# Kernel tuning notes

Measured on AMD Instinct MI355X. Metric: run time of the kernel, lower is better.

The kernel has to match this reference:

```python
import jax, jax.numpy as jnp
import numpy as np

N_NODES = 80_000
D_IN = 128
D_HID = 128
D_EMB = 64
N_EDGES = 2_560_000
NUM_PEAKS = 40_000
N_TF = 128
N_GENE = 8_000
MLP_HID = 128
N_OUT = 2


def setup_inputs() -> dict:
    key = jax.random.key(0)
    ks = jax.random.split(key, 8)
    x = jax.random.normal(ks[0], (N_NODES, D_IN), jnp.float32)
    edge_index = jax.random.randint(ks[1], (2, N_EDGES), 0, N_NODES)
    tf_index_list = jax.random.randint(ks[2], (N_TF,), 0, N_NODES - NUM_PEAKS)
    gene_index_list = jax.random.randint(ks[3], (N_GENE,), 0, N_NODES - NUM_PEAKS)
    s = lambda k, shp, fan: jax.random.normal(k, shp, jnp.float32) * np.float32(1.0 / np.sqrt(fan))
    W1 = s(ks[4], (D_IN, D_HID), D_IN)
    b1 = jnp.zeros((D_HID,), jnp.float32)
    W2 = s(ks[5], (D_HID, D_EMB), D_HID)
    b2 = jnp.zeros((D_EMB,), jnp.float32)
    Wm1 = s(ks[6], (2 * D_EMB, MLP_HID), 2 * D_EMB)
    bm1 = jnp.zeros((MLP_HID,), jnp.float32)
    Wm2 = s(ks[7], (MLP_HID, N_OUT), MLP_HID)
    bm2 = jnp.zeros((N_OUT,), jnp.float32)
    return dict(x=x, W1=W1, b1=b1, W2=W2, b2=b2, Wm1=Wm1, bm1=bm1, Wm2=Wm2, bm2=bm2,
                edge_index=edge_index, num=NUM_PEAKS,
                tf_index_list=tf_index_list, gene_index_list=gene_index_list)


def _gcn_agg(h, src, dst, n):
    # mean aggregation of neighbor features: agg[i] = mean_{(j->i) in E} h[j]
    deg = jax.ops.segment_sum(jnp.ones((src.shape[0],), h.dtype), dst, num_segments=n)
    agg = jax.ops.segment_sum(h[src], dst, num_segments=n)
    return agg / jnp.maximum(deg, 1.0)[:, None]


def reference(x, W1, b1, W2, b2, Wm1, bm1, Wm2, bm2,
              edge_index, num, tf_index_list, gene_index_list):
    src, dst = edge_index[0], edge_index[1]
    n = x.shape[0]
    # 2-layer GCN (mean aggregation) -> node embeddings [N, D_EMB]
    h = jax.nn.relu(_gcn_agg(x, src, dst, n) @ W1 + b1)
    emb = _gcn_agg(h, src, dst, n) @ W2 + b2
    # split_tensor(emb, num): pX = emb[:num] (unused), gX = emb[num:]
    gX = emb[num:]
    tf_emb = gX[tf_index_list]      # [T, d]
    g_emb = gX[gene_index_list]     # [G, d]
    T, d = tf_emb.shape
    G = g_emb.shape[0]
    # vectorized equivalent of the nested (tf, gene) concat loop; row order = tf*G + g
    combined = jnp.concatenate([
        jnp.broadcast_to(tf_emb[:, None, :], (T, G, d)),
        jnp.broadcast_to(g_emb[None, :, :], (T, G, d)),
    ], axis=-1).reshape(T * G, 2 * d)
    hid = jax.nn.relu(combined @ Wm1 + bm1)
    out = hid @ Wm2 + bm2
    return jax.nn.softmax(out, axis=-1)
```

## Files before the change

### kernel.cpp

```cpp
#include <hip/hip_runtime.h>
#include <math.h>

#define DIM 128
#define DEMB 64
#define CHUNK 8192


__device__ __forceinline__ unsigned pack_bf16x2(float a, float b) {
    unsigned ua = __float_as_uint(a);
    unsigned ub = __float_as_uint(b);
    ua = (ua + 0x7fffu + ((ua >> 16) & 1u)) >> 16;
    ub = (ub + 0x7fffu + ((ub >> 16) & 1u)) & 0xffff0000u;
    return ua | ub;
}
__device__ __forceinline__ float lo_bf16(unsigned v) { return __uint_as_float(v << 16); }
__device__ __forceinline__ float hi_bf16(unsigned v) { return __uint_as_float(v & 0xffff0000u); }


__global__ __launch_bounds__(256) void convert_kernel(const float* __restrict__ in,
                                                      unsigned* __restrict__ out, int n2) {
    int i = blockIdx.x * 256 + threadIdx.x;
    int stride = gridDim.x * 256;
    for (; i < n2; i += stride) {
        float2 v = reinterpret_cast<const float2*>(in)[i];
        out[i] = pack_bf16x2(v.x, v.y);
    }
}


__global__ __launch_bounds__(256) void bucket_count(const int* __restrict__ dst,
                                                    int* __restrict__ bcnt,
                                                    int n_edges, int nbuck) {
    __shared__ int h[384];
    for (int i = threadIdx.x; i < nbuck; i += 256) h[i] = 0;
    __syncthreads();
    int i = blockIdx.x * 256 + threadIdx.x;
    int stride = gridDim.x * 256;
    for (; i < n_edges; i += stride) atomicAdd(&h[dst[i] >> 8], 1);
    __syncthreads();
    for (int i2 = threadIdx.x; i2 < nbuck; i2 += 256)
        if (h[i2]) atomicAdd(&bcnt[i2], h[i2]);
}

__global__ __launch_bounds__(512) void bucket_scan(const int* __restrict__ bcnt,
                                                   int* __restrict__ bstart,
                                                   int* __restrict__ bcursor,
                                                   int nbuck, int n_edges) {
    __shared__ int sm[512];
    int tid = threadIdx.x;
    int v = (tid < nbuck) ? bcnt[tid] : 0;
    sm[tid] = v;
    __syncthreads();
    for (int off = 1; off < 512; off <<= 1) {
        int t = (tid >= off) ? sm[tid - off] : 0;
        __syncthreads();
        if (tid >= off) sm[tid] += t;
        __syncthreads();
    }
    if (tid < nbuck) {
        int e = sm[tid] - v;
        bstart[tid] = e;
        bcursor[tid] = e;
    }
    if (tid == 0) bstart[nbuck] = n_edges;
}

__global__ __launch_bounds__(256) void bucket_scatter(const int* __restrict__ src,
                                                      const int* __restrict__ dst,
                                                      int* __restrict__ bcursor,
                                                      unsigned* __restrict__ binned,
                                                      int n_edges, int nbuck) {
    __shared__ int cnt[384], off[384], gbase[384], cur[384];
    __shared__ unsigned stage[CHUNK];
    int tid = threadIdx.x;
    int e0 = blockIdx.x * CHUNK;
    int ne = min(CHUNK, n_edges - e0);
    for (int i = tid; i < nbuck; i += 256) cnt[i] = 0;
    __syncthreads();
    for (int j = tid; j < ne; j += 256) atomicAdd(&cnt[dst[e0 + j] >> 8], 1);
    __syncthreads();
    if (tid == 0) {
        int s = 0;
        for (int b = 0; b < nbuck; b++) { off[b] = s; s += cnt[b]; }
    }
    __syncthreads();
    for (int b = tid; b < nbuck; b += 256) {
        cur[b] = off[b];
        gbase[b] = cnt[b] ? atomicAdd(&bcursor[b], cnt[b]) : 0;
    }
    __syncthreads();
    for (int j = tid; j < ne; j += 256) {
        int d = dst[e0 + j];
        int s = src[e0 + j];
        int b = d >> 8;
        int p = atomicAdd(&cur[b], 1);
        stage[p] = ((unsigned)s << 8) | (unsigned)(d & 255);
    }
    __syncthreads();
    int wv = tid >> 6, lane = tid & 63;
    for (int b = wv; b < nbuck; b += 4) {
        int c = cnt[b], o = off[b], g = gbase[b];
        for (int k = lane; k < c; k += 64) binned[g + k] = stage[o + k];
    }
}

__global__ __launch_bounds__(256) void bucket_csr(const unsigned* __restrict__ binned,
                                                  const int* __restrict__ bstart,
                                                  int* __restrict__ counts,
                                                  int* __restrict__ rowstart,
                                                  int* __restrict__ ssorted,
                                                  int n_nodes) {
    __shared__ int sm[256], cur[256];
    __shared__ int cntv[256];
    int b = blockIdx.x;
    int bs = bstart[b], be = bstart[b + 1];
    int node0 = b << 8;
    int tid = threadIdx.x;
    cntv[tid] = 0;
    __syncthreads();
    for (int j = bs + tid; j < be; j += 256) atomicAdd(&cntv[binned[j] & 255u], 1);
    __syncthreads();
    int v = cntv[tid];
    sm[tid] = v;
    __syncthreads();
    for (int off = 1; off < 256; off <<= 1) {
        int t = (tid >= off) ? sm[tid - off] : 0;
        __syncthreads();
        if (tid >= off) sm[tid] += t;
        __syncthreads();
    }
    int excl = sm[tid] - v;
    int node = node0 + tid;
    if (node < n_nodes) {
        counts[node] = v;
        rowstart[node] = bs + excl;
    }
    cur[tid] = excl;
    __syncthreads();
    for (int j = bs + tid; j < be; j += 256) {
        unsigned e = binned[j];
        int p = atomicAdd(&cur[(int)(e & 255u)], 1);
        ssorted[bs + p] = (int)(e >> 8);
    }
}


__global__ __launch_bounds__(256) void agg_kernel(const unsigned* __restrict__ xh,
                                                  const int* __restrict__ rowstart,
                                                  const int* __restrict__ counts,
                                                  const int* __restrict__ ssorted,
                                                  float* __restrict__ A, int n_nodes) {
    int wave = (blockIdx.x * 256 + threadIdx.x) >> 6;
    int lane = threadIdx.x & 63;
    if (wave >= n_nodes) return;
    int base = rowstart[wave];
    int deg = counts[wave];
    const unsigned* xp = xh + lane;
    float ax = 0.f, ay = 0.f;
    int j = 0;
    for (; j + 8 <= deg; j += 8) {
        int s0 = ssorted[base + j];
        int s1 = ssorted[base + j + 1];
        int s2 = ssorted[base + j + 2];
        int s3 = ssorted[base + j + 3];
        int s4 = ssorted[base + j + 4];
        int s5 = ssorted[base + j + 5];
        int s6 = ssorted[base + j + 6];
        int s7 = ssorted[base + j + 7];
        unsigned v0 = xp[(size_t)s0 * 64];
        unsigned v1 = xp[(size_t)s1 * 64];
        unsigned v2 = xp[(size_t)s2 * 64];
        unsigned v3 = xp[(size_t)s3 * 64];
        unsigned v4 = xp[(size_t)s4 * 64];
        unsigned v5 = xp[(size_t)s5 * 64];
        unsigned v6 = xp[(size_t)s6 * 64];
        unsigned v7 = xp[(size_t)s7 * 64];
        ax += ((lo_bf16(v0) + lo_bf16(v1)) + (lo_bf16(v2) + lo_bf16(v3))) +
              ((lo_bf16(v4) + lo_bf16(v5)) + (lo_bf16(v6) + lo_bf16(v7)));
        ay += ((hi_bf16(v0) + hi_bf16(v1)) + (hi_bf16(v2) + hi_bf16(v3))) +
              ((hi_bf16(v4) + hi_bf16(v5)) + (hi_bf16(v6) + hi_bf16(v7)));
    }
    for (; j < deg; j++) {
        int s = ssorted[base + j];
        unsigned v = xp[(size_t)s * 64];
        ax += lo_bf16(v);
        ay += hi_bf16(v);
    }
    float inv = 1.f / fmaxf((float)deg, 1.f);
    float2 st = {ax * inv, ay * inv};
    *reinterpret_cast<float2*>(A + (size_t)wave * DIM + 2 * lane) = st;
}


__global__ __launch_bounds__(256) void gemm1_kernel(const float* __restrict__ A,
                                                    const float* __restrict__ W1,
                                                    const float* __restrict__ b1,
                                                    unsigned* __restrict__ Hh, int n_rows) {
    __shared__ float W1s[DIM * DIM];
    __shared__ float As[32 * DIM];
    int tid = threadIdx.x;
    for (int i = 0; i < 16; i++) {
        int idx = (i * 256 + tid) * 4;
        *reinterpret_cast<float4*>(&W1s[idx]) = *reinterpret_cast<const float4*>(&W1[idx]);
    }
    int r0 = blockIdx.x * 32;
    for (int i = 0; i < 4; i++) {
        int idx = (i * 256 + tid) * 4;
        int gr = r0 + (idx >> 7);
        float4 vv = {0, 0, 0, 0};
        if (gr < n_rows) vv = *reinterpret_cast<const float4*>(&A[(size_t)r0 * DIM + idx]);
        *reinterpret_cast<float4*>(&As[idx]) = vv;
    }
    __syncthreads();
    int tx = tid & 31, ty = tid >> 5;
    float4 b = *reinterpret_cast<const float4*>(&b1[tx * 4]);
    float acc[4][4];
#pragma unroll
    for (int i = 0; i < 4; i++) {
        acc[i][0] = b.x; acc[i][1] = b.y; acc[i][2] = b.z; acc[i][3] = b.w;
    }
#pragma unroll 8
    for (int kc = 0; kc < 32; kc++) {
        int k = kc * 4;
        float4 w0 = *reinterpret_cast<const float4*>(&W1s[(k + 0) * DIM + tx * 4]);
        float4 w1 = *reinterpret_cast<const float4*>(&W1s[(k + 1) * DIM + tx * 4]);
        float4 w2 = *reinterpret_cast<const float4*>(&W1s[(k + 2) * DIM + tx * 4]);
        float4 w3 = *reinterpret_cast<const float4*>(&W1s[(k + 3) * DIM + tx * 4]);
#pragma unroll
        for (int i = 0; i < 4; i++) {
            float4 a = *reinterpret_cast<const float4*>(&As[(ty * 4 + i) * DIM + k]);
            acc[i][0] += a.x * w0.x; acc[i][1] += a.x * w0.y; acc[i][2] += a.x * w0.z; acc[i][3] += a.x * w0.w;
            acc[i][0] += a.y * w1.x; acc[i][1] += a.y * w1.y; acc[i][2] += a.y * w1.z; acc[i][3] += a.y * w1.w;
            acc[i][0] += a.z * w2.x; acc[i][1] += a.z * w2.y; acc[i][2] += a.z * w2.z; acc[i][3] += a.z * w2.w;
            acc[i][0] += a.w * w3.x; acc[i][1] += a.w * w3.y; acc[i][2] += a.w * w3.z; acc[i][3] += a.w * w3.w;
        }
    }
#pragma unroll
    for (int i = 0; i < 4; i++) {
        int r = r0 + ty * 4 + i;
        if (r < n_rows) {
            float o0 = fmaxf(acc[i][0], 0.f);
            float o1 = fmaxf(acc[i][1], 0.f);
            float o2 = fmaxf(acc[i][2], 0.f);
            float o3 = fmaxf(acc[i][3], 0.f);
            uint2 pk = {pack_bf16x2(o0, o1), pack_bf16x2(o2, o3)};
            *reinterpret_cast<uint2*>(&Hh[(size_t)r * 64 + tx * 2]) = pk;
        }
    }
}


__global__ __launch_bounds__(256) void target_kernel(const unsigned* __restrict__ Hh,
                                                     const float* __restrict__ W2,
                                                     const float* __restrict__ b2,
                                                     const int* __restrict__ rowstart,
                                                     const int* __restrict__ counts,
                                                     const int* __restrict__ ssorted,
                                                     const int* __restrict__ dnum,
                                                     const int* __restrict__ tf_idx,
                                                     const int* __restrict__ gene_idx,
                                                     float* __restrict__ emb, int T, int ntar) {
    __shared__ float W2s[DIM * DEMB];
    __shared__ float aggS[4][DIM];
    int tid = threadIdx.x;
    for (int i = 0; i < 8; i++) {
        int idx = (i * 256 + tid) * 4;
        *reinterpret_cast<float4*>(&W2s[idx]) = *reinterpret_cast<const float4*>(&W2[idx]);
    }
    int wv = tid >> 6, lane = tid & 63;
    int i = blockIdx.x * 4 + wv;
    int num = dnum[0];
    if (i < ntar) {
        int idx = (i < T) ? tf_idx[i] : gene_idx[i - T];
        int node = num + idx;
        int base = rowstart[node];
        int deg = counts[node];
        const unsigned* hp = Hh + lane;
        float ax = 0.f, ay = 0.f;
        int j = 0;
        for (; j + 4 <= deg; j += 4) {
            int s0 = ssorted[base + j];
            int s1 = ssorted[base + j + 1];
            int s2 = ssorted[base + j + 2];
            int s3 = ssorted[base + j + 3];
            unsigned v0 = hp[(size_t)s0 * 64];
            unsigned v1 = hp[(size_t)s1 * 64];
            unsigned v2 = hp[(size_t)s2 * 64];
            unsigned v3 = hp[(size_t)s3 * 64];
            ax += (lo_bf16(v0) + lo_bf16(v1)) + (lo_bf16(v2) + lo_bf16(v3));
            ay += (hi_bf16(v0) + hi_bf16(v1)) + (hi_bf16(v2) + hi_bf16(v3));
        }
        for (; j < deg; j++) {
            int s = ssorted[base + j];
            unsigned v = hp[(size_t)s * 64];
            ax += lo_bf16(v);
            ay += hi_bf16(v);
        }
        float inv = 1.f / fmaxf((float)deg, 1.f);
        float2 st = {ax * inv, ay * inv};
        *reinterpret_cast<float2*>(&aggS[wv][2 * lane]) = st;
    }
    __syncthreads();
    if (i < ntar) {
        float e = b2[lane];
#pragma unroll 4
        for (int k = 0; k < DIM; k++) e += aggS[wv][k] * W2s[k * DEMB + lane];
        emb[(size_t)i * DEMB + lane] = e;
    }
}


__global__ __launch_bounds__(128) void ab_kernel(const float* __restrict__ emb,
                                                 const float* __restrict__ Wm1,
                                                 const float* __restrict__ bm1,
                                                 float* __restrict__ AB, int T, int ntar) {
    int i = blockIdx.x;
    int j = threadIdx.x;
    if (i >= ntar) return;
    const float* e = emb + (size_t)i * DEMB;
    int base = (i < T) ? 0 : DEMB;
    float acc = (i < T) ? bm1[j] : 0.f;
#pragma unroll 4
    for (int k = 0; k < DEMB; k++) acc += e[k] * Wm1[(size_t)(base + k) * DIM + j];
    AB[(size_t)i * DIM + j] = acc;
}


__global__ __launch_bounds__(256) void final_kernel(const float* __restrict__ AB,
                                                    const float* __restrict__ Wm2,
                                                    const float* __restrict__ bm2,
                                                    float* __restrict__ out, int T, int G) {
    __shared__ float tfAs[8 * DIM];
    __shared__ float wd[DIM];
    int tid = threadIdx.x;
    int t0 = blockIdx.y * 8;
    int g0 = blockIdx.x * 256;
    {
        int idx = tid * 4;
        int t = t0 + (idx >> 7);
        float4 v = {0, 0, 0, 0};
        if (t < T) v = *reinterpret_cast<const float4*>(&AB[(size_t)t0 * DIM + idx]);
        *reinterpret_cast<float4*>(&tfAs[idx]) = v;
    }
    if (tid < DIM) wd[tid] = Wm2[tid * 2] - Wm2[tid * 2 + 1];
    __syncthreads();
    int g = g0 + tid;
    int gc = min(g, G - 1);
    const float4* gp = reinterpret_cast<const float4*>(AB + (size_t)(T + gc) * DIM);
    float acc[8];
#pragma unroll
    for (int t = 0; t < 8; t++) acc[t] = 0.f;
    for (int kc = 0; kc < 16; kc++) {
        float4 ga = gp[kc * 2];
        float4 gb = gp[kc * 2 + 1];
        float4 wa = *reinterpret_cast<const float4*>(&wd[kc * 8]);
        float4 wb = *reinterpret_cast<const float4*>(&wd[kc * 8 + 4]);
#pragma unroll
        for (int t = 0; t < 8; t++) {
            const float4 ta = *reinterpret_cast<const float4*>(&tfAs[t * DIM + kc * 8]);
            const float4 tb = *reinterpret_cast<const float4*>(&tfAs[t * DIM + kc * 8 + 4]);
            acc[t] += fmaxf(ta.x + ga.x, 0.f) * wa.x;
            acc[t] += fmaxf(ta.y + ga.y, 0.f) * wa.y;
            acc[t] += fmaxf(ta.z + ga.z, 0.f) * wa.z;
            acc[t] += fmaxf(ta.w + ga.w, 0.f) * wa.w;
            acc[t] += fmaxf(tb.x + gb.x, 0.f) * wb.x;
            acc[t] += fmaxf(tb.y + gb.y, 0.f) * wb.y;
            acc[t] += fmaxf(tb.z + gb.z, 0.f) * wb.z;
            acc[t] += fmaxf(tb.w + gb.w, 0.f) * wb.w;
        }
    }
    if (g < G) {
        float bd = bm2[0] - bm2[1];
#pragma unroll
        for (int t = 0; t < 8; t++) {
            if (t0 + t < T) {
                float d = acc[t] + bd;
                float p0 = 1.f / (1.f + __expf(-d));
                float2 r = {p0, 1.f - p0};
                *reinterpret_cast<float2*>(&out[((size_t)(t0 + t) * G + g) * 2]) = r;
            }
        }
    }
}


extern "C" void kernel_launch(void* const* d_in, const int* in_sizes, int n_in,
                              void* d_out, int out_size, void* d_ws, size_t ws_size,
                              hipStream_t stream) {
    const float* x    = (const float*)d_in[0];
    const float* W1   = (const float*)d_in[1];
    const float* b1   = (const float*)d_in[2];
    const float* W2   = (const float*)d_in[3];
    const float* b2   = (const float*)d_in[4];
    const float* Wm1  = (const float*)d_in[5];
    const float* bm1  = (const float*)d_in[6];
    const float* Wm2  = (const float*)d_in[7];
    const float* bm2  = (const float*)d_in[8];
    const int* ei     = (const int*)d_in[9];
    const int* dnum   = (const int*)d_in[10];
    const int* tfidx  = (const int*)d_in[11];
    const int* geidx  = (const int*)d_in[12];
    float* out = (float*)d_out;

    int n_nodes = in_sizes[0] / DIM;
    int n_edges = in_sizes[9] / 2;
    int T = in_sizes[11];
    int G = in_sizes[12];
    int ntar = T + G;
    int nbuck = (n_nodes + 255) >> 8;
    const int* srcp = ei;
    const int* dstp = ei + n_edges;

    char* w = (char*)d_ws;
    size_t o = 0;
    auto alloc = [&](size_t bytes) {
        void* p = w + o;
        o += (bytes + 255) & ~(size_t)255;
        return p;
    };
    unsigned* xh   = (unsigned*)alloc((size_t)n_nodes * 64 * 4);
    unsigned* Hh   = (unsigned*)alloc((size_t)n_nodes * 64 * 4);
    float* A       = (float*)alloc((size_t)n_nodes * DIM * 4);
    int* ssorted   = (int*)alloc((size_t)n_edges * 4);
    int* counts    = (int*)alloc((size_t)n_nodes * 4);
    int* rowstart  = (int*)alloc((size_t)n_nodes * 4);
    int* bcnt      = (int*)alloc(2048);
    int* bstart    = (int*)alloc(2048);
    int* bcursor   = (int*)alloc(2048);
    unsigned* binned = Hh;
    float* emb = A;
    float* AB  = A + (8u * 1024u * 1024u / 4u);

    hipMemsetAsync(bcnt, 0, (size_t)nbuck * 4, stream);

    convert_kernel<<<2048, 256, 0, stream>>>(x, xh, n_nodes * 64);
    bucket_count<<<256, 256, 0, stream>>>(dstp, bcnt, n_edges, nbuck);
    bucket_scan<<<1, 512, 0, stream>>>(bcnt, bstart, bcursor, nbuck, n_edges);
    bucket_scatter<<<(n_edges + CHUNK - 1) / CHUNK, 256, 0, stream>>>(srcp, dstp, bcursor,
                                                                      binned, n_edges, nbuck);
    bucket_csr<<<nbuck, 256, 0, stream>>>(binned, bstart, counts, rowstart, ssorted, n_nodes);

    agg_kernel<<<(n_nodes + 3) / 4, 256, 0, stream>>>(xh, rowstart, counts, ssorted, A, n_nodes);
    gemm1_kernel<<<(n_nodes + 31) / 32, 256, 0, stream>>>(A, W1, b1, Hh, n_nodes);
    target_kernel<<<(ntar + 3) / 4, 256, 0, stream>>>(Hh, W2, b2, rowstart, counts, ssorted,
                                                      dnum, tfidx, geidx, emb, T, ntar);
    ab_kernel<<<ntar, 128, 0, stream>>>(emb, Wm1, bm1, AB, T, ntar);
    final_kernel<<<dim3((G + 255) / 256, (T + 7) / 8), 256, 0, stream>>>(AB, Wm2, bm2, out, T, G);
}
```

Before: 421.1 us.

## Store aggregated features as bf16, parallelize bucket scan and flatten scatter writeback

The first-layer aggregate is now written as packed bf16 instead of fp32, so gemm1 reads half as many bytes and both the write and the read traffic shrink. In bucket_scatter, the serial single-thread prefix sum is replaced by a two-pass block-wide Hillis-Steele scan. The per-bucket wave copy-out is replaced by a flat per-element writeback that uses a stored bucket id. bucket_count also gets more blocks. The cost is an extra bf16 rounding of the aggregated activations, about 16KB more shared memory in the scatter kernel, and emb/AB now sit at a smaller offset inside a smaller buffer.

```diff
diff --git a/kernel.cpp b/kernel.cpp
--- a/kernel.cpp
+++ b/kernel.cpp
@@ -70,8 +70,11 @@
                                                       int* __restrict__ bcursor,
                                                       unsigned* __restrict__ binned,
                                                       int n_edges, int nbuck) {
+    __shared__ unsigned stage[CHUNK];
+    __shared__ unsigned short bkt[CHUNK];
     __shared__ int cnt[384], off[384], gbase[384], cur[384];
-    __shared__ unsigned stage[CHUNK];
+    __shared__ int sc[256];
+    __shared__ int tot0;
     int tid = threadIdx.x;
     int e0 = blockIdx.x * CHUNK;
     int ne = min(CHUNK, n_edges - e0);
@@ -79,11 +82,32 @@
     __syncthreads();
     for (int j = tid; j < ne; j += 256) atomicAdd(&cnt[dst[e0 + j] >> 8], 1);
     __syncthreads();
-    if (tid == 0) {
-        int s = 0;
-        for (int b = 0; b < nbuck; b++) { off[b] = s; s += cnt[b]; }
-    }
-    __syncthreads();
+    {
+        int v0 = (tid < nbuck) ? cnt[tid] : 0;
+        sc[tid] = v0;
+        __syncthreads();
+        for (int o = 1; o < 256; o <<= 1) {
+            int t = (tid >= o) ? sc[tid - o] : 0;
+            __syncthreads();
+            sc[tid] += t;
+            __syncthreads();
+        }
+        if (tid < nbuck) off[tid] = sc[tid] - v0;
+        if (tid == 255) tot0 = sc[255];
+        __syncthreads();
+        int i1 = 256 + tid;
+        int v1 = (i1 < nbuck) ? cnt[i1] : 0;
+        sc[tid] = v1;
+        __syncthreads();
+        for (int o = 1; o < 256; o <<= 1) {
+            int t = (tid >= o) ? sc[tid - o] : 0;
+            __syncthreads();
+            sc[tid] += t;
+            __syncthreads();
+        }
+        if (i1 < nbuck) off[i1] = tot0 + sc[tid] - v1;
+        __syncthreads();
+    }
     for (int b = tid; b < nbuck; b += 256) {
         cur[b] = off[b];
         gbase[b] = cnt[b] ? atomicAdd(&bcursor[b], cnt[b]) : 0;
@@ -95,12 +119,12 @@
         int b = d >> 8;
         int p = atomicAdd(&cur[b], 1);
         stage[p] = ((unsigned)s << 8) | (unsigned)(d & 255);
-    }
-    __syncthreads();
-    int wv = tid >> 6, lane = tid & 63;
-    for (int b = wv; b < nbuck; b += 4) {
-        int c = cnt[b], o = off[b], g = gbase[b];
-        for (int k = lane; k < c; k += 64) binned[g + k] = stage[o + k];
+        bkt[p] = (unsigned short)b;
+    }
+    __syncthreads();
+    for (int j = tid; j < ne; j += 256) {
+        int b = bkt[j];
+        binned[gbase[b] + (j - off[b])] = stage[j];
     }
 }
 
@@ -149,7 +173,7 @@
                                                   const int* __restrict__ rowstart,
                                                   const int* __restrict__ counts,
                                                   const int* __restrict__ ssorted,
-                                                  float* __restrict__ A, int n_nodes) {
+                                                  unsigned* __restrict__ Ah, int n_nodes) {
     int wave = (blockIdx.x * 256 + threadIdx.x) >> 6;
     int lane = threadIdx.x & 63;
     if (wave >= n_nodes) return;
@@ -187,29 +211,28 @@
         ay += hi_bf16(v);
     }
     float inv = 1.f / fmaxf((float)deg, 1.f);
-    float2 st = {ax * inv, ay * inv};
-    *reinterpret_cast<float2*>(A + (size_t)wave * DIM + 2 * lane) = st;
-}
-
-
-__global__ __launch_bounds__(256) void gemm1_kernel(const float* __restrict__ A,
+    Ah[(size_t)wave * 64 + lane] = pack_bf16x2(ax * inv, ay * inv);
+}
+
+
+__global__ __launch_bounds__(256) void gemm1_kernel(const unsigned* __restrict__ Ah,
                                                     const float* __restrict__ W1,
                                                     const float* __restrict__ b1,
                                                     unsigned* __restrict__ Hh, int n_rows) {
     __shared__ float W1s[DIM * DIM];
-    __shared__ float As[32 * DIM];
+    __shared__ unsigned As[32 * 64];
     int tid = threadIdx.x;
     for (int i = 0; i < 16; i++) {
         int idx = (i * 256 + tid) * 4;
         *reinterpret_cast<float4*>(&W1s[idx]) = *reinterpret_cast<const float4*>(&W1[idx]);
     }
     int r0 = blockIdx.x * 32;
-    for (int i = 0; i < 4; i++) {
+    for (int i = 0; i < 2; i++) {
         int idx = (i * 256 + tid) * 4;
-        int gr = r0 + (idx >> 7);
-        float4 vv = {0, 0, 0, 0};
-        if (gr < n_rows) vv = *reinterpret_cast<const float4*>(&A[(size_t)r0 * DIM + idx]);
-        *reinterpret_cast<float4*>(&As[idx]) = vv;
+        int gr = r0 + (idx >> 6);
+        uint4 vv = {0, 0, 0, 0};
+        if (gr < n_rows) vv = *reinterpret_cast<const uint4*>(&Ah[(size_t)r0 * 64 + idx]);
+        *reinterpret_cast<uint4*>(&As[idx]) = vv;
     }
     __syncthreads();
     int tx = tid & 31, ty = tid >> 5;
@@ -228,11 +251,13 @@
         float4 w3 = *reinterpret_cast<const float4*>(&W1s[(k + 3) * DIM + tx * 4]);
 #pragma unroll
         for (int i = 0; i < 4; i++) {
-            float4 a = *reinterpret_cast<const float4*>(&As[(ty * 4 + i) * DIM + k]);
-            acc[i][0] += a.x * w0.x; acc[i][1] += a.x * w0.y; acc[i][2] += a.x * w0.z; acc[i][3] += a.x * w0.w;
-            acc[i][0] += a.y * w1.x; acc[i][1] += a.y * w1.y; acc[i][2] += a.y * w1.z; acc[i][3] += a.y * w1.w;
-            acc[i][0] += a.z * w2.x; acc[i][1] += a.z * w2.y; acc[i][2] += a.z * w2.z; acc[i][3] += a.z * w2.w;
-            acc[i][0] += a.w * w3.x; acc[i][1] += a.w * w3.y; acc[i][2] += a.w * w3.z; acc[i][3] += a.w * w3.w;
+            uint2 av = *reinterpret_cast<const uint2*>(&As[(ty * 4 + i) * 64 + kc * 2]);
+            float a0 = lo_bf16(av.x), a1 = hi_bf16(av.x);
+            float a2 = lo_bf16(av.y), a3 = hi_bf16(av.y);
+            acc[i][0] += a0 * w0.x; acc[i][1] += a0 * w0.y; acc[i][2] += a0 * w0.z; acc[i][3] += a0 * w0.w;
+            acc[i][0] += a1 * w1.x; acc[i][1] += a1 * w1.y; acc[i][2] += a1 * w1.z; acc[i][3] += a1 * w1.w;
+            acc[i][0] += a2 * w2.x; acc[i][1] += a2 * w2.y; acc[i][2] += a2 * w2.z; acc[i][3] += a2 * w2.w;
+            acc[i][0] += a3 * w3.x; acc[i][1] += a3 * w3.y; acc[i][2] += a3 * w3.z; acc[i][3] += a3 * w3.w;
         }
     }
 #pragma unroll
@@ -420,7 +445,7 @@
     };
     unsigned* xh   = (unsigned*)alloc((size_t)n_nodes * 64 * 4);
     unsigned* Hh   = (unsigned*)alloc((size_t)n_nodes * 64 * 4);
-    float* A       = (float*)alloc((size_t)n_nodes * DIM * 4);
+    unsigned* Ah   = (unsigned*)alloc((size_t)n_nodes * 64 * 4);
     int* ssorted   = (int*)alloc((size_t)n_edges * 4);
     int* counts    = (int*)alloc((size_t)n_nodes * 4);
     int* rowstart  = (int*)alloc((size_t)n_nodes * 4);
@@ -428,20 +453,20 @@
     int* bstart    = (int*)alloc(2048);
     int* bcursor   = (int*)alloc(2048);
     unsigned* binned = Hh;
-    float* emb = A;
-    float* AB  = A + (8u * 1024u * 1024u / 4u);
+    float* emb = (float*)Ah;
+    float* AB  = (float*)Ah + (4u * 1024u * 1024u / 4u);
 
     hipMemsetAsync(bcnt, 0, (size_t)nbuck * 4, stream);
 
     convert_kernel<<<2048, 256, 0, stream>>>(x, xh, n_nodes * 64);
-    bucket_count<<<256, 256, 0, stream>>>(dstp, bcnt, n_edges, nbuck);
+    bucket_count<<<1024, 256, 0, stream>>>(dstp, bcnt, n_edges, nbuck);
     bucket_scan<<<1, 512, 0, stream>>>(bcnt, bstart, bcursor, nbuck, n_edges);
     bucket_scatter<<<(n_edges + CHUNK - 1) / CHUNK, 256, 0, stream>>>(srcp, dstp, bcursor,
                                                                       binned, n_edges, nbuck);
     bucket_csr<<<nbuck, 256, 0, stream>>>(binned, bstart, counts, rowstart, ssorted, n_nodes);
 
-    agg_kernel<<<(n_nodes + 3) / 4, 256, 0, stream>>>(xh, rowstart, counts, ssorted, A, n_nodes);
-    gemm1_kernel<<<(n_nodes + 31) / 32, 256, 0, stream>>>(A, W1, b1, Hh, n_nodes);
+    agg_kernel<<<(n_nodes + 3) / 4, 256, 0, stream>>>(xh, rowstart, counts, ssorted, Ah, n_nodes);
+    gemm1_kernel<<<(n_nodes + 31) / 32, 256, 0, stream>>>(Ah, W1, b1, Hh, n_nodes);
     target_kernel<<<(ntar + 3) / 4, 256, 0, stream>>>(Hh, W2, b2, rowstart, counts, ssorted,
                                                       dnum, tfidx, geidx, emb, T, ntar);
     ab_kernel<<<ntar, 128, 0, stream>>>(emb, Wm1, bm1, AB, T, ntar);
```

After: 411.6 us. 2.2% less time.
